# Kernel tuning notes

Measured on AMD Instinct MI355X. Metric: run time of the kernel, lower is better.

## Reference

```python
import jax, jax.numpy as jnp
import numpy as np

NUM_EXPERTS = 8
TOP_K = 2

def setup_inputs() -> dict:
    key = jax.random.key(0)
    ks = jax.random.split(key, 7)
    T, D, H, E = 4096, 1024, 4096, NUM_EXPERTS
    s_in = (2.0 / (D + H)) ** 0.5   # xavier-ish scale for W1
    s_out = (2.0 / (H + D)) ** 0.5
    return {
        "x": jax.random.normal(ks[0], (T, D), jnp.float32),
        "Wg": jax.random.normal(ks[1], (D, E), jnp.float32) * 0.02,
        "bg": jnp.zeros((E,), jnp.float32),
        "W1": jax.random.normal(ks[2], (E, D, H), jnp.float32) * s_in,
        "b1": jnp.zeros((E, H), jnp.float32),
        "W2": jax.random.normal(ks[3], (E, H, D), jnp.float32) * s_out,
        "b2": jnp.zeros((E, D), jnp.float32),
    }

def reference(x, Wg, bg, W1, b1, W2, b2):
    # x: [T, D]; gate over E experts
    gate = jax.nn.softmax(x @ Wg + bg, axis=-1)            # [T, E]
    _, top_idx = jax.lax.top_k(gate, TOP_K)                # [T, K]
    # mask[t, e] = True iff expert e is among top-k for token t
    mask = jnp.any(top_idx[:, :, None] == jnp.arange(NUM_EXPERTS)[None, None, :], axis=1)
    combine_w = jnp.where(mask, gate, 0.0)                 # [T, E]
    # out = sum_e combine_w[:, e] * MLP_e(x); non-selected tokens get weight 0
    out = jnp.zeros_like(x)
    for e in range(NUM_EXPERTS):  # small fixed expert loop
        h = jax.nn.relu(x @ W1[e] + b1[e])                 # [T, H]
        y = h @ W2[e] + b2[e]                              # [T, D]
        out = out + combine_w[:, e:e + 1] * y
    return out
```

## Files before the change

kernel.cpp:

```cpp
#include <hip/hip_runtime.h>
#include <stdint.h>

#define T_TOK 4096
#define DDIM  1024
#define HDIM  4096
#define NEXP  8
#define MAXTILES 72

typedef short s16x8  __attribute__((ext_vector_type(8)));
typedef float f32x4t __attribute__((ext_vector_type(4)));

#define GLOAD16(gp, lp) __builtin_amdgcn_global_load_lds( \
    (const __attribute__((address_space(1))) unsigned int*)(gp), \
    (__attribute__((address_space(3))) unsigned int*)(lp), 16, 0, 0)
#define SB0 __builtin_amdgcn_sched_barrier(0)

__device__ __forceinline__ unsigned short f2b(float f){
  unsigned int u = __float_as_uint(f);
  u += 0x7fffu + ((u >> 16) & 1u);
  return (unsigned short)(u >> 16);
}

__device__ __forceinline__ s16x8 lds_frag(const unsigned short* base, int row, int colElem){
  int byte = row*64 + ((colElem*2) ^ (((row >> 1) & 3) << 4));
  return *(const s16x8*)((const char*)base + byte);
}

__global__ void gate_kernel(const float* __restrict__ x, const float* __restrict__ Wg,
                            const float* __restrict__ bg,
                            int* __restrict__ topk_e, float* __restrict__ topk_w,
                            unsigned short* __restrict__ xb){
  const int t = blockIdx.x;
  const int lane = threadIdx.x;
  const float* xr = x + (size_t)t * DDIM;
  unsigned short* xbr = xb + (size_t)t * DDIM;
  float acc[NEXP];
  #pragma unroll
  for (int e = 0; e < NEXP; ++e) acc[e] = 0.f;
  #pragma unroll 4
  for (int it = 0; it < DDIM/64; ++it){
    int i = it*64 + lane;
    float xi = xr[i];
    xbr[i] = f2b(xi);
    const float4* wr = (const float4*)(Wg + (size_t)i * NEXP);
    float4 w0 = wr[0], w1 = wr[1];
    acc[0] += xi*w0.x; acc[1] += xi*w0.y; acc[2] += xi*w0.z; acc[3] += xi*w0.w;
    acc[4] += xi*w1.x; acc[5] += xi*w1.y; acc[6] += xi*w1.z; acc[7] += xi*w1.w;
  }
  #pragma unroll
  for (int e = 0; e < NEXP; ++e){
    float v = acc[e];
    #pragma unroll
    for (int off = 32; off > 0; off >>= 1) v += __shfl_xor(v, off, 64);
    acc[e] = v;
  }
  if (lane == 0){
    float l[NEXP], m = -1e30f;
    #pragma unroll
    for (int e = 0; e < NEXP; ++e){ l[e] = acc[e] + bg[e]; m = fmaxf(m, l[e]); }
    float p[NEXP], s = 0.f;
    #pragma unroll
    for (int e = 0; e < NEXP; ++e){ p[e] = expf(l[e] - m); s += p[e]; }
    float inv = 1.f / s;
    int a1 = 0; float v1 = -1.f;
    #pragma unroll
    for (int e = 0; e < NEXP; ++e){ p[e] *= inv; if (p[e] > v1){ v1 = p[e]; a1 = e; } }
    int a2 = -1; float v2 = -1.f;
    #pragma unroll
    for (int e = 0; e < NEXP; ++e){ if (e == a1) continue; if (p[e] > v2){ v2 = p[e]; a2 = e; } }
    topk_e[2*t]   = a1; topk_w[2*t]   = v1;
    topk_e[2*t+1] = a2; topk_w[2*t+1] = v2;
  }
}

__global__ void route_count(const int* __restrict__ topk_e, const float* __restrict__ topk_w,
                            int* __restrict__ expertList, float* __restrict__ pairW,
                            int* __restrict__ counts){
  const int e = blockIdx.x;
  const int tid = threadIdx.x;
  __shared__ int pfx[256];
  __shared__ int base_s;
  if (tid == 0) base_s = 0;
  __syncthreads();
  for (int c = 0; c < T_TOK/256; ++c){
    int t = c*256 + tid;
    int e0 = topk_e[2*t], e1 = topk_e[2*t+1];
    int sel = 0; float w = 0.f;
    if (e0 == e){ sel = 1; w = topk_w[2*t]; }
    else if (e1 == e){ sel = 1; w = topk_w[2*t+1]; }
    pfx[tid] = sel;
    __syncthreads();
    for (int off = 1; off < 256; off <<= 1){
      int v = (tid >= off) ? pfx[tid - off] : 0;
      __syncthreads();
      pfx[tid] += v;
      __syncthreads();
    }
    if (sel){
      int pos = base_s + pfx[tid] - 1;
      expertList[e*T_TOK + pos] = t;
      pairW[e*T_TOK + pos] = w;
    }
    __syncthreads();
    if (tid == 0) base_s += pfx[255];
    __syncthreads();
  }
  if (tid == 0) counts[e] = base_s;
}

__global__ void plan_kernel(const int* __restrict__ counts, int* __restrict__ nTiles,
                            int* __restrict__ tileExpert, int* __restrict__ tileStart){
  if (blockIdx.x != 0 || threadIdx.x != 0) return;
  int nt = 0;
  for (int e = 0; e < NEXP; ++e){
    int c = counts[e];
    int tcount = (c + 127) >> 7;
    for (int i = 0; i < tcount; ++i){ tileExpert[nt] = e; tileStart[nt] = i*128; ++nt; }
  }
  *nTiles = nt;
}

__global__ __launch_bounds__(256)
void transpose_w(const float* __restrict__ W, unsigned short* __restrict__ Wt,
                 int K, int N){
  const int e = blockIdx.z;
  const float* Wb = W + (size_t)e*K*N;
  unsigned short* Wtb = Wt + (size_t)e*K*N;
  const int n0 = blockIdx.x*64, k0 = blockIdx.y*64;
  __shared__ unsigned short t[64][72];
  const int r  = threadIdx.x >> 4;
  const int c4 = (threadIdx.x & 15) * 4;
  #pragma unroll
  for (int i = 0; i < 4; ++i){
    int k = r + i*16;
    float4 v = *(const float4*)(Wb + (size_t)(k0+k)*N + n0 + c4);
    t[c4+0][k] = f2b(v.x); t[c4+1][k] = f2b(v.y);
    t[c4+2][k] = f2b(v.z); t[c4+3][k] = f2b(v.w);
  }
  __syncthreads();
  const int kk = (threadIdx.x & 7) * 8;
  #pragma unroll
  for (int i = 0; i < 2; ++i){
    int n = (threadIdx.x >> 3) + i*32;
    s16x8 v;
    #pragma unroll
    for (int j = 0; j < 8; ++j) v[j] = (short)t[n][kk+j];
    *(s16x8*)(Wtb + (size_t)(n0+n)*K + k0 + kk) = v;
  }
}

template<int LAYER, int KS>
__global__ __launch_bounds__(256, 4)
void moe_gemm(const unsigned short* __restrict__ Abf,
              const unsigned short* __restrict__ Wt,
              const float* __restrict__ bias,
              const int* __restrict__ nTilesPtr,
              const int* __restrict__ tileExpert,
              const int* __restrict__ tileStart,
              const int* __restrict__ counts,
              const int* __restrict__ expertList,
              const float* __restrict__ pairW,
              unsigned short* __restrict__ Hout,
              float* __restrict__ out)
{
  constexpr int KD = (LAYER == 1) ? DDIM : HDIM;
  constexpr int ND = (LAYER == 1) ? HDIM : DDIM;
  constexpr int NB = ND / 128;
  constexpr int NTfull = KD / 32;

  const int nwg = gridDim.x;
  const int b   = blockIdx.x;
  const int q8 = nwg >> 3, r8 = nwg & 7;
  const int xcd = b & 7, ii = b >> 3;
  const int lin = (xcd < r8 ? xcd*(q8+1) : r8*(q8+1) + (xcd-r8)*q8) + ii;
  const int tile = lin / NB;
  const int n0   = (lin % NB) * 128;
  const int kz   = blockIdx.y;

  if (tile >= *nTilesPtr) return;
  const int e   = tileExpert[tile];
  const int ts  = tileStart[tile];
  const int cnt = counts[e];
  const int tid  = threadIdx.x;
  const int lane = tid & 63;
  const int wave = tid >> 6;
  const int wm = (wave >> 1) * 64;
  const int wn = (wave & 1) * 64;

  __shared__ __align__(16) unsigned short As[2][128][32];
  __shared__ __align__(16) unsigned short Bs[2][128][32];
  __shared__ int   tokenBuf[128];
  __shared__ float wBuf[128];

  if (tid < 128){
    int pos = ts + tid;
    int tok = 0; float w = 0.f;
    if (pos < cnt){ tok = expertList[e*T_TOK + pos]; w = pairW[e*T_TOK + pos]; }
    tokenBuf[tid] = tok; wBuf[tid] = w;
  }
  __syncthreads();

  const int srow = tid >> 2;
  const int slot = (tid & 3) ^ ((tid >> 3) & 3);
  const int koff = slot * 8;
  const unsigned short* gA[2];
  const unsigned short* gB[2];
  #pragma unroll
  for (int g = 0; g < 2; ++g){
    const int row = g*64 + srow;
    if (LAYER == 1) gA[g] = Abf + (size_t)tokenBuf[row]*DDIM + koff;
    else            gA[g] = Abf + (size_t)(tile*128 + row)*HDIM + koff;
    gB[g] = Wt + ((size_t)e*ND + n0 + row)*KD + koff;
  }

  auto STAGE = [&](int buf, int ko){
    unsigned short* la = &As[buf][wave*16][0];
    unsigned short* lb = &Bs[buf][wave*16][0];
    #pragma unroll
    for (int g = 0; g < 2; ++g){
      GLOAD16(gA[g] + ko, la + g*2048);
      GLOAD16(gB[g] + ko, lb + g*2048);
    }
  };

  f32x4t acc[4][4] = {};
  const int fr = lane & 15;
  const int fq = lane >> 4;

  const int kt0 = (kz * NTfull) / KS;
  const int kt1 = ((kz + 1) * NTfull) / KS;
  const int NTl = kt1 - kt0;

  STAGE(0, kt0*32);

  int cur = 0;
  for (int t = 0; t < NTl; ++t){
    if (t + 1 < NTl){
      STAGE(cur ^ 1, (kt0 + t + 1)*32);
      SB0; asm volatile("s_waitcnt vmcnt(4)" ::: "memory");
    } else {
      SB0; asm volatile("s_waitcnt vmcnt(0)" ::: "memory");
    }
    __builtin_amdgcn_s_barrier();
    SB0;

    const unsigned short* Ab = &As[cur][0][0];
    const unsigned short* Bb = &Bs[cur][0][0];
    s16x8 bfr[4], afr[4];
    #pragma unroll
    for (int nf = 0; nf < 4; ++nf) bfr[nf] = lds_frag(Bb, wn + nf*16 + fr, fq*8);
    #pragma unroll
    for (int mf = 0; mf < 4; ++mf) afr[mf] = lds_frag(Ab, wm + mf*16 + fr, fq*8);
    #pragma unroll
    for (int mf = 0; mf < 4; ++mf)
      #pragma unroll
      for (int nf = 0; nf < 4; ++nf)
        acc[mf][nf] = __builtin_amdgcn_mfma_f32_16x16x32_bf16(afr[mf], bfr[nf], acc[mf][nf], 0, 0, 0);

    SB0;
    __builtin_amdgcn_s_barrier();
    SB0;
    cur ^= 1;
  }

  const int rbase = wm + fq*4;
  const int cbase = wn + fr;
  if (LAYER == 1){
    #pragma unroll
    for (int mf = 0; mf < 4; ++mf){
      #pragma unroll
      for (int nf = 0; nf < 4; ++nf){
        int c = cbase + nf*16;
        float bsv = bias[e*HDIM + n0 + c];
        #pragma unroll
        for (int j = 0; j < 4; ++j){
          int rr = rbase + mf*16 + j;
          float v = fmaxf(acc[mf][nf][j] + bsv, 0.f);
          __builtin_nontemporal_store((unsigned short)f2b(v),
              &Hout[(size_t)(tile*128 + rr)*HDIM + n0 + c]);
        }
      }
    }
  } else {
    #pragma unroll
    for (int mf = 0; mf < 4; ++mf){
      #pragma unroll
      for (int j = 0; j < 4; ++j){
        int rr = rbase + mf*16 + j;
        if (ts + rr < cnt){
          int tok = tokenBuf[rr];
          float w = wBuf[rr];
          #pragma unroll
          for (int nf = 0; nf < 4; ++nf){
            int c = cbase + nf*16;
            float v = acc[mf][nf][j];
            if (kz == 0) v += bias[e*DDIM + n0 + c];
            atomicAdd(out + (size_t)tok*DDIM + n0 + c, w * v);
          }
        }
      }
    }
  }
}

extern "C" void kernel_launch(void* const* d_in, const int* in_sizes, int n_in,
                              void* d_out, int out_size, void* d_ws, size_t ws_size,
                              hipStream_t stream){
  const float* x  = (const float*)d_in[0];
  const float* Wg = (const float*)d_in[1];
  const float* bg = (const float*)d_in[2];
  const float* W1 = (const float*)d_in[3];
  const float* b1 = (const float*)d_in[4];
  const float* W2 = (const float*)d_in[5];
  const float* b2 = (const float*)d_in[6];
  float* out = (float*)d_out;

  char* p = (char*)d_ws;
  int*   topk_e     = (int*)p;   p += (size_t)T_TOK*2*sizeof(int);
  float* topk_w     = (float*)p; p += (size_t)T_TOK*2*sizeof(float);
  int*   counts     = (int*)p;   p += 8*sizeof(int);
  int*   nTiles     = (int*)p;   p += 8*sizeof(int);
  int*   tileExpert = (int*)p;   p += 128*sizeof(int);
  int*   tileStart  = (int*)p;   p += 128*sizeof(int);
  int*   expertList = (int*)p;   p += (size_t)NEXP*T_TOK*sizeof(int);
  float* pairW      = (float*)p; p += (size_t)NEXP*T_TOK*sizeof(float);
  p = (char*)(((uintptr_t)p + 255) & ~(uintptr_t)255);
  unsigned short* xb = (unsigned short*)p;
  p += (size_t)T_TOK*DDIM*sizeof(unsigned short);
  p = (char*)(((uintptr_t)p + 255) & ~(uintptr_t)255);
  unsigned short* Wtbuf = (unsigned short*)p;
  p += (size_t)NEXP*DDIM*HDIM*sizeof(unsigned short);
  p = (char*)(((uintptr_t)p + 255) & ~(uintptr_t)255);
  unsigned short* Hact = (unsigned short*)p;

  hipMemsetAsync(d_out, 0, (size_t)T_TOK*DDIM*sizeof(float), stream);
  gate_kernel<<<T_TOK, 64, 0, stream>>>(x, Wg, bg, topk_e, topk_w, xb);
  route_count<<<NEXP, 256, 0, stream>>>(topk_e, topk_w, expertList, pairW, counts);
  plan_kernel<<<1, 1, 0, stream>>>(counts, nTiles, tileExpert, tileStart);

  transpose_w<<<dim3(HDIM/64, DDIM/64, NEXP), 256, 0, stream>>>(W1, Wtbuf, DDIM, HDIM);
  moe_gemm<1,1><<<dim3(MAXTILES*(HDIM/128), 1), 256, 0, stream>>>(
      xb, Wtbuf, b1, nTiles, tileExpert, tileStart, counts, expertList, pairW, Hact, nullptr);

  transpose_w<<<dim3(DDIM/64, HDIM/64, NEXP), 256, 0, stream>>>(W2, Wtbuf, HDIM, DDIM);
  moe_gemm<2,2><<<dim3(MAXTILES*(DDIM/128), 2), 256, 0, stream>>>(
      Hact, Wtbuf, b2, nTiles, tileExpert, tileStart, counts, expertList, pairW, nullptr, out);
}
```

Before: 384.3 us.

## Overlap weight transposes with routing and GEMM1 via fused launches

Fuses the W1 transpose into the routing kernel's grid and the W2 transpose into the GEMM1 grid, with extra blocks doing transpose work, so weight conversion overlaps with routing and compute instead of running as separate serial launches. This needs a separate W2t buffer, so the fused path runs only when the workspace is large enough and otherwise falls back to the old sequence. It also adds a dedicated GEMM1 kernel with XCD-aware tile remapping and nontemporal stores. The cost is larger grids and transpose blocks competing with GEMM blocks for CUs and bandwidth.

```diff
diff --git a/kernel.cpp b/kernel.cpp
--- a/kernel.cpp
+++ b/kernel.cpp
@@ -6,6 +6,8 @@
 #define HDIM  4096
 #define NEXP  8
 #define MAXTILES 72
+#define G1_NWG (MAXTILES*(HDIM/128))
+#define TW_NWG 8192
 
 typedef short s16x8  __attribute__((ext_vector_type(8)));
 typedef float f32x4t __attribute__((ext_vector_type(4)));
@@ -24,6 +26,37 @@
 __device__ __forceinline__ s16x8 lds_frag(const unsigned short* base, int row, int colElem){
   int byte = row*64 + ((colElem*2) ^ (((row >> 1) & 3) << 4));
   return *(const s16x8*)((const char*)base + byte);
+}
+
+__device__ __forceinline__ void transpose_body(const float* __restrict__ W,
+                                               unsigned short* __restrict__ Wt,
+                                               int K, int N, int bid, int tid,
+                                               unsigned short (*t)[72]){
+  const int nb = N >> 6, kb = K >> 6;
+  const int n0 = (bid % nb) * 64;
+  const int k0 = ((bid / nb) % kb) * 64;
+  const int e  = bid / (nb * kb);
+  const float* Wb = W + (size_t)e*K*N;
+  unsigned short* Wtb = Wt + (size_t)e*K*N;
+  const int r  = tid >> 4;
+  const int c4 = (tid & 15) * 4;
+  #pragma unroll
+  for (int i = 0; i < 4; ++i){
+    int k = r + i*16;
+    float4 v = *(const float4*)(Wb + (size_t)(k0+k)*N + n0 + c4);
+    t[c4+0][k] = f2b(v.x); t[c4+1][k] = f2b(v.y);
+    t[c4+2][k] = f2b(v.z); t[c4+3][k] = f2b(v.w);
+  }
+  __syncthreads();
+  const int kk = (tid & 7) * 8;
+  #pragma unroll
+  for (int i = 0; i < 2; ++i){
+    int n = (tid >> 3) + i*32;
+    s16x8 v;
+    #pragma unroll
+    for (int j = 0; j < 8; ++j) v[j] = (short)t[n][kk+j];
+    *(s16x8*)(Wtb + (size_t)(n0+n)*K + k0 + kk) = v;
+  }
 }
 
 __global__ void gate_kernel(const float* __restrict__ x, const float* __restrict__ Wg,
@@ -73,14 +106,13 @@
   }
 }
 
-__global__ void route_count(const int* __restrict__ topk_e, const float* __restrict__ topk_w,
-                            int* __restrict__ expertList, float* __restrict__ pairW,
-                            int* __restrict__ counts){
-  const int e = blockIdx.x;
-  const int tid = threadIdx.x;
-  __shared__ int pfx[256];
-  __shared__ int base_s;
-  if (tid == 0) base_s = 0;
+__device__ __forceinline__ void route_body(const int* __restrict__ topk_e,
+                                           const float* __restrict__ topk_w,
+                                           int* __restrict__ expertList,
+                                           float* __restrict__ pairW,
+                                           int* __restrict__ counts,
+                                           int e, int tid, int* pfx, int* base_s){
+  if (tid == 0) *base_s = 0;
   __syncthreads();
   for (int c = 0; c < T_TOK/256; ++c){
     int t = c*256 + tid;
@@ -97,15 +129,40 @@
       __syncthreads();
     }
     if (sel){
-      int pos = base_s + pfx[tid] - 1;
+      int pos = *base_s + pfx[tid] - 1;
       expertList[e*T_TOK + pos] = t;
       pairW[e*T_TOK + pos] = w;
     }
     __syncthreads();
-    if (tid == 0) base_s += pfx[255];
+    if (tid == 0) *base_s += pfx[255];
     __syncthreads();
   }
-  if (tid == 0) counts[e] = base_s;
+  if (tid == 0) counts[e] = *base_s;
+}
+
+__global__ __launch_bounds__(256)
+void route_count(const int* __restrict__ topk_e, const float* __restrict__ topk_w,
+                 int* __restrict__ expertList, float* __restrict__ pairW,
+                 int* __restrict__ counts){
+  __shared__ int pfx[256];
+  __shared__ int base_s;
+  route_body(topk_e, topk_w, expertList, pairW, counts, blockIdx.x, threadIdx.x, pfx, &base_s);
+}
+
+__global__ __launch_bounds__(256)
+void route_t1_fused(const int* __restrict__ topk_e, const float* __restrict__ topk_w,
+                    int* __restrict__ expertList, float* __restrict__ pairW,
+                    int* __restrict__ counts,
+                    const float* __restrict__ W1, unsigned short* __restrict__ W1t){
+  __shared__ __align__(16) unsigned char smem[9216];
+  if (blockIdx.x < NEXP){
+    int* pfx = (int*)smem;
+    int* base_s = (int*)(smem + 1024);
+    route_body(topk_e, topk_w, expertList, pairW, counts, blockIdx.x, threadIdx.x, pfx, base_s);
+  } else {
+    transpose_body(W1, W1t, DDIM, HDIM, blockIdx.x - NEXP, threadIdx.x,
+                   (unsigned short (*)[72])smem);
+  }
 }
 
 __global__ void plan_kernel(const int* __restrict__ counts, int* __restrict__ nTiles,
@@ -123,30 +180,9 @@
 __global__ __launch_bounds__(256)
 void transpose_w(const float* __restrict__ W, unsigned short* __restrict__ Wt,
                  int K, int N){
-  const int e = blockIdx.z;
-  const float* Wb = W + (size_t)e*K*N;
-  unsigned short* Wtb = Wt + (size_t)e*K*N;
-  const int n0 = blockIdx.x*64, k0 = blockIdx.y*64;
   __shared__ unsigned short t[64][72];
-  const int r  = threadIdx.x >> 4;
-  const int c4 = (threadIdx.x & 15) * 4;
-  #pragma unroll
-  for (int i = 0; i < 4; ++i){
-    int k = r + i*16;
-    float4 v = *(const float4*)(Wb + (size_t)(k0+k)*N + n0 + c4);
-    t[c4+0][k] = f2b(v.x); t[c4+1][k] = f2b(v.y);
-    t[c4+2][k] = f2b(v.z); t[c4+3][k] = f2b(v.w);
-  }
-  __syncthreads();
-  const int kk = (threadIdx.x & 7) * 8;
-  #pragma unroll
-  for (int i = 0; i < 2; ++i){
-    int n = (threadIdx.x >> 3) + i*32;
-    s16x8 v;
-    #pragma unroll
-    for (int j = 0; j < 8; ++j) v[j] = (short)t[n][kk+j];
-    *(s16x8*)(Wtb + (size_t)(n0+n)*K + k0 + kk) = v;
-  }
+  const int bid = blockIdx.x + blockIdx.y*gridDim.x + blockIdx.z*gridDim.x*gridDim.y;
+  transpose_body(W, Wt, K, N, bid, threadIdx.x, t);
 }
 
 template<int LAYER, int KS>
@@ -303,6 +339,136 @@
   }
 }
 
+__global__ __launch_bounds__(256, 4)
+void gemm1_t2_fused(const unsigned short* __restrict__ Abf,
+                    const unsigned short* __restrict__ Wt,
+                    const float* __restrict__ bias,
+                    const int* __restrict__ nTilesPtr,
+                    const int* __restrict__ tileExpert,
+                    const int* __restrict__ tileStart,
+                    const int* __restrict__ counts,
+                    const int* __restrict__ expertList,
+                    unsigned short* __restrict__ Hout,
+                    const float* __restrict__ W2,
+                    unsigned short* __restrict__ W2t)
+{
+  __shared__ __align__(16) unsigned char smem[33792];
+  if (blockIdx.x >= G1_NWG){
+    transpose_body(W2, W2t, HDIM, DDIM, blockIdx.x - G1_NWG, threadIdx.x,
+                   (unsigned short (*)[72])smem);
+    return;
+  }
+  auto As = (unsigned short (*)[128][32])smem;
+  auto Bs = (unsigned short (*)[128][32])(smem + 16384);
+  int* tokenBuf = (int*)(smem + 32768);
+
+  constexpr int KD = DDIM, ND = HDIM;
+  constexpr int NB = ND / 128;
+  constexpr int NT = KD / 32;
+
+  const int nwg = G1_NWG;
+  const int b   = blockIdx.x;
+  const int q8 = nwg >> 3, r8 = nwg & 7;
+  const int xcd = b & 7, ii = b >> 3;
+  const int lin = (xcd < r8 ? xcd*(q8+1) : r8*(q8+1) + (xcd-r8)*q8) + ii;
+  const int tile = lin / NB;
+  const int n0   = (lin % NB) * 128;
+
+  if (tile >= *nTilesPtr) return;
+  const int e   = tileExpert[tile];
+  const int ts  = tileStart[tile];
+  const int cnt = counts[e];
+  const int tid  = threadIdx.x;
+  const int lane = tid & 63;
+  const int wave = tid >> 6;
+  const int wm = (wave >> 1) * 64;
+  const int wn = (wave & 1) * 64;
+
+  if (tid < 128){
+    int pos = ts + tid;
+    int tok = 0;
+    if (pos < cnt) tok = expertList[e*T_TOK + pos];
+    tokenBuf[tid] = tok;
+  }
+  __syncthreads();
+
+  const int srow = tid >> 2;
+  const int slot = (tid & 3) ^ ((tid >> 3) & 3);
+  const int koff = slot * 8;
+  const unsigned short* gA[2];
+  const unsigned short* gB[2];
+  #pragma unroll
+  for (int g = 0; g < 2; ++g){
+    const int row = g*64 + srow;
+    gA[g] = Abf + (size_t)tokenBuf[row]*DDIM + koff;
+    gB[g] = Wt + ((size_t)e*ND + n0 + row)*KD + koff;
+  }
+
+  auto STAGE = [&](int buf, int ko){
+    unsigned short* la = &As[buf][wave*16][0];
+    unsigned short* lb = &Bs[buf][wave*16][0];
+    #pragma unroll
+    for (int g = 0; g < 2; ++g){
+      GLOAD16(gA[g] + ko, la + g*2048);
+      GLOAD16(gB[g] + ko, lb + g*2048);
+    }
+  };
+
+  f32x4t acc[4][4] = {};
+  const int fr = lane & 15;
+  const int fq = lane >> 4;
+
+  STAGE(0, 0);
+
+  int cur = 0;
+  for (int t = 0; t < NT; ++t){
+    if (t + 1 < NT){
+      STAGE(cur ^ 1, (t + 1)*32);
+      SB0; asm volatile("s_waitcnt vmcnt(4)" ::: "memory");
+    } else {
+      SB0; asm volatile("s_waitcnt vmcnt(0)" ::: "memory");
+    }
+    __builtin_amdgcn_s_barrier();
+    SB0;
+
+    const unsigned short* Ab = &As[cur][0][0];
+    const unsigned short* Bb = &Bs[cur][0][0];
+    s16x8 bfr[4], afr[4];
+    #pragma unroll
+    for (int nf = 0; nf < 4; ++nf) bfr[nf] = lds_frag(Bb, wn + nf*16 + fr, fq*8);
+    #pragma unroll
+    for (int mf = 0; mf < 4; ++mf) afr[mf] = lds_frag(Ab, wm + mf*16 + fr, fq*8);
+    #pragma unroll
+    for (int mf = 0; mf < 4; ++mf)
+      #pragma unroll
+      for (int nf = 0; nf < 4; ++nf)
+        acc[mf][nf] = __builtin_amdgcn_mfma_f32_16x16x32_bf16(afr[mf], bfr[nf], acc[mf][nf], 0, 0, 0);
+
+    SB0;
+    __builtin_amdgcn_s_barrier();
+    SB0;
+    cur ^= 1;
+  }
+
+  const int rbase = wm + fq*4;
+  const int cbase = wn + fr;
+  #pragma unroll
+  for (int mf = 0; mf < 4; ++mf){
+    #pragma unroll
+    for (int nf = 0; nf < 4; ++nf){
+      int c = cbase + nf*16;
+      float bsv = bias[e*HDIM + n0 + c];
+      #pragma unroll
+      for (int j = 0; j < 4; ++j){
+        int rr = rbase + mf*16 + j;
+        float v = fmaxf(acc[mf][nf][j] + bsv, 0.f);
+        __builtin_nontemporal_store((unsigned short)f2b(v),
+            &Hout[(size_t)(tile*128 + rr)*HDIM + n0 + c]);
+      }
+    }
+  }
+}
+
 extern "C" void kernel_launch(void* const* d_in, const int* in_sizes, int n_in,
                               void* d_out, int out_size, void* d_ws, size_t ws_size,
                               hipStream_t stream){
@@ -314,6 +480,9 @@
   const float* W2 = (const float*)d_in[5];
   const float* b2 = (const float*)d_in[6];
   float* out = (float*)d_out;
+
+  const size_t WB = (size_t)NEXP*DDIM*HDIM*sizeof(unsigned short);
+  const size_t HB = (size_t)MAXTILES*128*HDIM*sizeof(unsigned short);
 
   char* p = (char*)d_ws;
   int*   topk_e     = (int*)p;   p += (size_t)T_TOK*2*sizeof(int);
@@ -328,21 +497,39 @@
   unsigned short* xb = (unsigned short*)p;
   p += (size_t)T_TOK*DDIM*sizeof(unsigned short);
   p = (char*)(((uintptr_t)p + 255) & ~(uintptr_t)255);
-  unsigned short* Wtbuf = (unsigned short*)p;
-  p += (size_t)NEXP*DDIM*HDIM*sizeof(unsigned short);
+  unsigned short* W1t = (unsigned short*)p; p += WB;
   p = (char*)(((uintptr_t)p + 255) & ~(uintptr_t)255);
+
+  const size_t used = (size_t)(p - (char*)d_ws);
+  const bool sep = (used + WB + 256 + HB + 256) <= ws_size;
+  unsigned short* W2t;
+  if (sep){
+    W2t = (unsigned short*)p; p += WB;
+    p = (char*)(((uintptr_t)p + 255) & ~(uintptr_t)255);
+  } else {
+    W2t = W1t;
+  }
   unsigned short* Hact = (unsigned short*)p;
 
   hipMemsetAsync(d_out, 0, (size_t)T_TOK*DDIM*sizeof(float), stream);
   gate_kernel<<<T_TOK, 64, 0, stream>>>(x, Wg, bg, topk_e, topk_w, xb);
-  route_count<<<NEXP, 256, 0, stream>>>(topk_e, topk_w, expertList, pairW, counts);
-  plan_kernel<<<1, 1, 0, stream>>>(counts, nTiles, tileExpert, tileStart);
-
-  transpose_w<<<dim3(HDIM/64, DDIM/64, NEXP), 256, 0, stream>>>(W1, Wtbuf, DDIM, HDIM);
-  moe_gemm<1,1><<<dim3(MAXTILES*(HDIM/128), 1), 256, 0, stream>>>(
-      xb, Wtbuf, b1, nTiles, tileExpert, tileStart, counts, expertList, pairW, Hact, nullptr);
-
-  transpose_w<<<dim3(DDIM/64, HDIM/64, NEXP), 256, 0, stream>>>(W2, Wtbuf, HDIM, DDIM);
-  moe_gemm<2,2><<<dim3(MAXTILES*(DDIM/128), 2), 256, 0, stream>>>(
-      Hact, Wtbuf, b2, nTiles, tileExpert, tileStart, counts, expertList, pairW, nullptr, out);
-}
+
+  if (sep){
+    route_t1_fused<<<NEXP + TW_NWG, 256, 0, stream>>>(
+        topk_e, topk_w, expertList, pairW, counts, W1, W1t);
+    plan_kernel<<<1, 1, 0, stream>>>(counts, nTiles, tileExpert, tileStart);
+    gemm1_t2_fused<<<G1_NWG + TW_NWG, 256, 0, stream>>>(
+        xb, W1t, b1, nTiles, tileExpert, tileStart, counts, expertList, Hact, W2, W2t);
+    moe_gemm<2,2><<<dim3(MAXTILES*(DDIM/128), 2), 256, 0, stream>>>(
+        Hact, W2t, b2, nTiles, tileExpert, tileStart, counts, expertList, pairW, nullptr, out);
+  } else {
+    route_count<<<NEXP, 256, 0, stream>>>(topk_e, topk_w, expertList, pairW, counts);
+    plan_kernel<<<1, 1, 0, stream>>>(counts, nTiles, tileExpert, tileStart);
+    transpose_w<<<dim3(HDIM/64, DDIM/64, NEXP), 256, 0, stream>>>(W1, W1t, DDIM, HDIM);
+    moe_gemm<1,1><<<dim3(G1_NWG, 1), 256, 0, stream>>>(
+        xb, W1t, b1, nTiles, tileExpert, tileStart, counts, expertList, pairW, Hact, nullptr);
+    transpose_w<<<dim3(DDIM/64, HDIM/64, NEXP), 256, 0, stream>>>(W2, W1t, HDIM, DDIM);
+    moe_gemm<2,2><<<dim3(MAXTILES*(DDIM/128), 2), 256, 0, stream>>>(
+        Hact, W1t, b2, nTiles, tileExpert, tileStart, counts, expertList, pairW, nullptr, out);
+  }
+}
```

Result: faster. 373.4 us (-2.8%).
